# Optimization experiments

Measured on AMD Instinct MI355X. Metric: run time of the kernel, lower is better.

Reference implementation:

```python
import jax, jax.numpy as jnp
import numpy as np

NF, LF, D_E, D_R = 32, 9, 200, 200
N_ENT, B = 100000, 1024
EPS = 1e-5


def _bn(x, gamma, beta, axes):
    # training-mode batchnorm: biased variance over `axes`
    m = jnp.mean(x, axis=axes, keepdims=True)
    v = jnp.var(x, axis=axes, keepdims=True)
    return (x - m) * jax.lax.rsqrt(v + EPS) * gamma + beta


def setup_inputs() -> dict:
    key = jax.random.key(0)
    ks = jax.random.split(key, 8)
    fc1_len = NF * LF                      # 288
    fc_len = (D_E - LF + 1) * NF           # 6144
    return {
        "e1": jax.random.normal(ks[0], (B, D_E), jnp.float32),
        "r": jax.random.normal(ks[1], (B, D_R), jnp.float32),
        "fc1_w": jax.random.normal(ks[2], (fc1_len, D_R), jnp.float32) * 0.05,
        "fc1_b": jnp.zeros((fc1_len,), jnp.float32),
        "fc_w": jax.random.normal(ks[3], (D_E, fc_len), jnp.float32) * 0.02,
        "fc_b": jnp.zeros((D_E,), jnp.float32),
        "E": jax.random.normal(ks[4], (N_ENT, D_E), jnp.float32) * 0.05,
        "b": jnp.zeros((N_ENT,), jnp.float32),
        "bn0_g": jnp.ones((1,), jnp.float32),
        "bn0_b": jnp.zeros((1,), jnp.float32),
        "bn1_g": jnp.ones((NF,), jnp.float32),
        "bn1_b": jnp.zeros((NF,), jnp.float32),
        "bn2_g": jnp.ones((D_E,), jnp.float32),
        "bn2_b": jnp.zeros((D_E,), jnp.float32),
    }


def reference(e1, r, fc1_w, fc1_b, fc_w, fc_b, E, b,
              bn0_g, bn0_b, bn1_g, bn1_b, bn2_g, bn2_b):
    L = D_E - LF + 1                       # 192 output positions
    # bn0 over [B,1,d_e]: normalize across batch and length (1 channel)
    x = _bn(e1[:, None, :], bn0_g[None, :, None], bn0_b[None, :, None], (0, 2))
    x = x[:, 0, :]                         # [B, d_e]
    # hypernetwork: per-sample conv filters [B, nf, lf]
    k = (r @ fc1_w.T + fc1_b).reshape(B, NF, LF)
    # grouped conv1d (groups=B) == per-sample sliding-window contraction
    idx = jnp.arange(L)[:, None] + jnp.arange(LF)[None, :]   # [L, lf]
    Xw = x[:, idx]                          # [B, L, lf] windows
    conv = jnp.einsum('blj,bfj->bfl', Xw, k)  # [B, nf, L]
    # bn1 over channels nf
    y = _bn(conv, bn1_g[None, :, None], bn1_b[None, :, None], (0, 2))
    y = y.reshape(B, NF * L)
    y = y @ fc_w.T + fc_b                   # [B, d_e]
    y = _bn(y, bn2_g[None, :], bn2_b[None, :], (0,))
    y = jax.nn.relu(y)
    scores = y @ E.T + b                    # [B, n_ent]
    return jax.nn.sigmoid(scores)
```

## Files before the change

kernel.cpp:

```cpp
#include <hip/hip_runtime.h>
#include <math.h>

#define B_    1024
#define DE    200
#define DR    200
#define NFC   32
#define LFC   9
#define LL    192
#define FC1LEN 288
#define FCLEN 6144
#define NENT  100000
#define EPSI  1e-5f
#define KPAD  224
#define NKS   7
#define YKS   192
#define YSEG  16

#define O_S0    0
#define O_P0    64
#define O_S1    256
#define O_S2    320
#define O_P1    768
#define O_RBF   66304
#define O_W1BF  180992
#define O_K     213248
#define O_CFRAG 508160
#define O_FCWP  3653888
#define O_CVEC  4440320
#define O_PART  4440576
#define O_Y     7717376
#define O_ABF   7922176

typedef __attribute__((ext_vector_type(8))) short bf16x8;
typedef __attribute__((ext_vector_type(4))) float f32x4;

__device__ __forceinline__ float sigm(float x){
  return __fdividef(1.0f, 1.0f + __expf(-x));
}

__device__ __forceinline__ unsigned short f2bf(float f){
  unsigned int u = __float_as_uint(f);
  u = (u + 0x7FFFu + ((u >> 16) & 1u)) >> 16;
  return (unsigned short)u;
}

__device__ __forceinline__ bf16x8 pack8(float4 f0, float4 f1){
  bf16x8 o;
  o[0]=(short)f2bf(f0.x); o[1]=(short)f2bf(f0.y); o[2]=(short)f2bf(f0.z); o[3]=(short)f2bf(f0.w);
  o[4]=(short)f2bf(f1.x); o[5]=(short)f2bf(f1.y); o[6]=(short)f2bf(f1.z); o[7]=(short)f2bf(f1.w);
  return o;
}

__global__ void k_bn0_part(const float* __restrict__ e1, float* __restrict__ ws){
  __shared__ float ss[256], sq[256];
  int tid = threadIdx.x;
  float a = 0.f, b = 0.f;
  for (int i = blockIdx.x*256 + tid; i < B_*DE; i += 64*256){
    float v = e1[i]; a += v; b += v*v;
  }
  ss[tid]=a; sq[tid]=b; __syncthreads();
  for (int s=128; s>0; s>>=1){
    if (tid < s){ ss[tid]+=ss[tid+s]; sq[tid]+=sq[tid+s]; }
    __syncthreads();
  }
  if (tid==0){ ws[O_P0+2*blockIdx.x]=ss[0]; ws[O_P0+2*blockIdx.x+1]=sq[0]; }
}

__global__ void k_bn0_final(const float* __restrict__ g, const float* __restrict__ bt,
                            float* __restrict__ ws){
  int tid = threadIdx.x;
  float a = ws[O_P0+2*tid], b = ws[O_P0+2*tid+1];
  for (int o=32; o>0; o>>=1){ a += __shfl_down(a,o); b += __shfl_down(b,o); }
  if (tid==0){
    float n = (float)(B_*DE);
    float m = a/n, v = b/n - m*m;
    float s = rsqrtf(v + EPSI) * g[0];
    ws[O_S0]   = s;
    ws[O_S0+1] = bt[0] - m*s;
  }
}

__global__ void k_pack(const float* __restrict__ r, const float* __restrict__ w,
                       float* __restrict__ ws){
  int blk = blockIdx.x;
  if (blk < 112){
    int s = blk*256 + threadIdx.x;
    int lane = s & 63;
    int ks = (s >> 6) % NKS;
    int mtile = (s >> 6) / NKS;
    int m = mtile*16 + (lane & 15);
    int k0 = ks*32 + (lane >> 4)*8;
    unsigned short o8[8];
    #pragma unroll
    for (int j = 0; j < 8; ++j){
      int k = k0 + j;
      o8[j] = f2bf((k < DR) ? r[m*DR + k] : 0.f);
    }
    *(bf16x8*)((unsigned short*)(ws + O_RBF) + (size_t)s*8) = *(bf16x8*)o8;
  } else {
    int s = (blk-112)*256 + threadIdx.x;
    if (s >= 18*NKS*64) return;
    int lane = s & 63;
    int ks = (s >> 6) % NKS;
    int ntile = (s >> 6) / NKS;
    int n = ntile*16 + (lane & 15);
    int k0 = ks*32 + (lane >> 4)*8;
    unsigned short o8[8];
    #pragma unroll
    for (int j = 0; j < 8; ++j){
      int k = k0 + j;
      o8[j] = f2bf((k < DR) ? w[(size_t)n*DR + k] : 0.f);
    }
    *(bf16x8*)((unsigned short*)(ws + O_W1BF) + (size_t)s*8) = *(bf16x8*)o8;
  }
}

__global__ void k_fc1m(const float* __restrict__ bias, float* __restrict__ ws){
  const unsigned short* Rb = (const unsigned short*)(ws + O_RBF);
  const unsigned short* Wb = (const unsigned short*)(ws + O_W1BF);
  int mt = blockIdx.x;
  int nt = blockIdx.y;
  int lane = threadIdx.x;
  int lr = lane & 15, lg = lane >> 4;
  f32x4 acc[4] = {};
  #pragma unroll
  for (int ks = 0; ks < NKS; ++ks){
    bf16x8 b = *(const bf16x8*)(Wb + ((size_t)(nt*NKS + ks)*64 + lane)*8);
    #pragma unroll
    for (int mf = 0; mf < 4; ++mf){
      bf16x8 a = *(const bf16x8*)(Rb + ((size_t)((mt*4+mf)*NKS + ks)*64 + lane)*8);
      acc[mf] = __builtin_amdgcn_mfma_f32_16x16x32_bf16(a, b, acc[mf], 0, 0, 0);
    }
  }
  int col = nt*16 + lr;
  float bv = bias[col];
  #pragma unroll
  for (int mf = 0; mf < 4; ++mf){
    int row = mt*64 + mf*16 + lg*4;
    #pragma unroll
    for (int r = 0; r < 4; ++r)
      ws[O_K + (size_t)(row + r)*FC1LEN + col] = acc[mf][r] + bv;
  }
}

__global__ void k_conv(const float* __restrict__ e1, float* __restrict__ ws){
  __shared__ float xs[DE];
  __shared__ float kf[FC1LEN];
  int b = blockIdx.x, tid = threadIdx.x;
  float s0v = ws[O_S0], t0v = ws[O_S0+1];
  for (int d = tid; d < DE;     d += 256) xs[d] = e1[b*DE + d]*s0v + t0v;
  for (int i = tid; i < FC1LEN; i += 256) kf[i] = ws[O_K + (size_t)b*FC1LEN + i];
  __syncthreads();
  unsigned short* Cf = (unsigned short*)(ws + O_CFRAG);
  int f = tid >> 3, sub = tid & 7;
  int mtile = b >> 4, mlan = b & 15;
  float kr[LFC];
  #pragma unroll
  for (int j = 0; j < LFC; ++j) kr[j] = kf[f*LFC + j];
  float sum = 0.f, sq = 0.f;
  #pragma unroll
  for (int g = 0; g < 3; ++g){
    unsigned short o8[8];
    int l0 = sub*24 + g*8;
    #pragma unroll
    for (int t = 0; t < 8; ++t){
      int l = l0 + t;
      float acc = 0.f;
      #pragma unroll
      for (int j = 0; j < LFC; ++j) acc += xs[l+j]*kr[j];
      o8[t] = f2bf(acc);
      sum += acc; sq += acc*acc;
    }
    int k0 = f*LL + l0;
    int ks = k0 >> 5;
    int lane_w = ((k0 >> 3) & 3)*16 + mlan;
    size_t slot = (size_t)(mtile*YKS + ks)*64 + lane_w;
    *(bf16x8*)(Cf + slot*8) = *(bf16x8*)o8;
  }
  for (int o = 1; o < 8; o <<= 1){ sum += __shfl_xor(sum,o); sq += __shfl_xor(sq,o); }
  if (sub == 0){
    ws[O_P1 + (b*NFC + f)*2    ] = sum;
    ws[O_P1 + (b*NFC + f)*2 + 1] = sq;
  }
}

__global__ void k_bn1_final(const float* __restrict__ g, const float* __restrict__ bt,
                            float* __restrict__ ws){
  __shared__ float ss[256], sq[256];
  int f = blockIdx.x, tid = threadIdx.x;
  float a = 0.f, b = 0.f;
  for (int i = tid; i < B_; i += 256){
    a += ws[O_P1 + (i*NFC + f)*2];
    b += ws[O_P1 + (i*NFC + f)*2 + 1];
  }
  ss[tid]=a; sq[tid]=b; __syncthreads();
  for (int s=128; s>0; s>>=1){
    if (tid < s){ ss[tid]+=ss[tid+s]; sq[tid]+=sq[tid+s]; }
    __syncthreads();
  }
  if (tid==0){
    float n = (float)(B_*LL);
    float m = ss[0]/n, v = sq[0]/n - m*m;
    float s = rsqrtf(v + EPSI) * g[f];
    ws[O_S1 + f]       = s;
    ws[O_S1 + NFC + f] = bt[f] - m*s;
  }
}

__global__ void k_fcwp(const float* __restrict__ fcw, float* __restrict__ ws){
  int s = blockIdx.x*256 + threadIdx.x;
  int lane = s & 63;
  int ks = (s >> 6) % YKS;
  int ntile = (s >> 6) / YKS;
  int n = ntile*16 + (lane & 15);
  int k0 = ks*32 + (lane >> 4)*8;
  int f = (k0 >> 6) / 3;
  float sc = ws[O_S1 + f];
  unsigned short o8[8];
  if (n < DE){
    const float* p = fcw + (size_t)n*FCLEN + k0;
    float4 f0 = *(const float4*)p;
    float4 f1 = *(const float4*)(p + 4);
    o8[0]=f2bf(f0.x*sc); o8[1]=f2bf(f0.y*sc); o8[2]=f2bf(f0.z*sc); o8[3]=f2bf(f0.w*sc);
    o8[4]=f2bf(f1.x*sc); o8[5]=f2bf(f1.y*sc); o8[6]=f2bf(f1.z*sc); o8[7]=f2bf(f1.w*sc);
  } else {
    #pragma unroll
    for (int j = 0; j < 8; ++j) o8[j] = 0;
  }
  *(bf16x8*)((unsigned short*)(ws + O_FCWP) + (size_t)s*8) = *(bf16x8*)o8;
}

__global__ void k_cvec(const float* __restrict__ fcw, const float* __restrict__ fcb,
                       float* __restrict__ ws){
  __shared__ float t1s[NFC];
  __shared__ float red[256];
  int o = blockIdx.x, tid = threadIdx.x;
  if (tid < NFC) t1s[tid] = ws[O_S1 + NFC + tid];
  __syncthreads();
  float acc = 0.f;
  for (int i = tid; i < FCLEN; i += 256)
    acc += fcw[(size_t)o*FCLEN + i] * t1s[i/LL];
  red[tid] = acc; __syncthreads();
  for (int s=128; s>0; s>>=1){
    if (tid < s) red[tid] += red[tid+s];
    __syncthreads();
  }
  if (tid==0) ws[O_CVEC + o] = red[0] + fcb[o];
}

__global__ __launch_bounds__(256) void k_ygemm_m(float* __restrict__ ws){
  const unsigned short* Cb = (const unsigned short*)(ws + O_CFRAG);
  const unsigned short* Wb = (const unsigned short*)(ws + O_FCWP);
  int mt = blockIdx.x;
  int seg = blockIdx.y;
  int tid = threadIdx.x;
  int lane = tid & 63, wid = tid >> 6;
  int lr = lane & 15, lg = lane >> 4;
  f32x4 acc[4][4] = {};
  #pragma unroll 4
  for (int ksl = 0; ksl < 12; ++ksl){
    int ks = seg*12 + ksl;
    bf16x8 a[4], bfr[4];
    #pragma unroll
    for (int mf = 0; mf < 4; ++mf)
      a[mf] = *(const bf16x8*)(Cb + ((size_t)((mt*4+mf)*YKS + ks)*64 + lane)*8);
    #pragma unroll
    for (int nf = 0; nf < 4; ++nf){
      int nt = wid*4 + nf;
      bfr[nf] = *(const bf16x8*)(Wb + ((size_t)(nt*YKS + ks)*64 + lane)*8);
    }
    #pragma unroll
    for (int mf = 0; mf < 4; ++mf)
      #pragma unroll
      for (int nf = 0; nf < 4; ++nf)
        acc[mf][nf] = __builtin_amdgcn_mfma_f32_16x16x32_bf16(a[mf], bfr[nf], acc[mf][nf], 0, 0, 0);
  }
  float* part = ws + O_PART + (size_t)seg*(B_*DE);
  #pragma unroll
  for (int nf = 0; nf < 4; ++nf){
    int col = (wid*4 + nf)*16 + lr;
    if (col < DE){
      #pragma unroll
      for (int mf = 0; mf < 4; ++mf){
        int row = mt*64 + mf*16 + lg*4;
        #pragma unroll
        for (int r = 0; r < 4; ++r)
          part[(size_t)(row + r)*DE + col] = acc[mf][nf][r];
      }
    }
  }
}

__global__ void k_yreduce(float* __restrict__ ws){
  int i = blockIdx.x*256 + threadIdx.x;
  int o = i % DE;
  float y = ws[O_CVEC + o];
  #pragma unroll
  for (int s = 0; s < YSEG; ++s) y += ws[O_PART + (size_t)s*(B_*DE) + i];
  ws[O_Y + i] = y;
}

__global__ void k_bn2(const float* __restrict__ g, const float* __restrict__ bt,
                      float* __restrict__ ws){
  __shared__ float ss[256], sq[256];
  int o = blockIdx.x, tid = threadIdx.x;
  float a = 0.f, b = 0.f;
  for (int i = tid; i < B_; i += 256){
    float v = ws[O_Y + i*DE + o];
    a += v; b += v*v;
  }
  ss[tid]=a; sq[tid]=b; __syncthreads();
  for (int s=128; s>0; s>>=1){
    if (tid < s){ ss[tid]+=ss[tid+s]; sq[tid]+=sq[tid+s]; }
    __syncthreads();
  }
  if (tid==0){
    float n = (float)B_;
    float m = ss[0]/n, v = sq[0]/n - m*m;
    float s = rsqrtf(v + EPSI) * g[o];
    ws[O_S2 + o]      = s;
    ws[O_S2 + DE + o] = bt[o] - m*s;
  }
}

__global__ void k_abf(float* __restrict__ ws){
  int s = blockIdx.x*256 + threadIdx.x;
  int lane = s & 63;
  int ks = (s >> 6) % NKS;
  int mtile = (s >> 6) / NKS;
  int m = mtile*16 + (lane & 15);
  int k0 = ks*32 + (lane >> 4)*8;
  unsigned short o8[8];
  #pragma unroll
  for (int j = 0; j < 8; ++j){
    int k = k0 + j;
    float v = 0.f;
    if (k < DE){
      float y = ws[O_Y + m*DE + k];
      v = fmaxf(y*ws[O_S2 + k] + ws[O_S2 + DE + k], 0.f);
    }
    o8[j] = f2bf(v);
  }
  *(bf16x8*)((unsigned short*)(ws + O_ABF) + (size_t)s*8) = *(bf16x8*)o8;
}

__global__ __launch_bounds__(256, 2) void k_scores(const float* __restrict__ E,
                                                   const float* __restrict__ bias,
                                                   const float* __restrict__ ws,
                                                   float* __restrict__ out){
  __shared__ float tile[64*256];
  const unsigned short* Abf = (const unsigned short*)(ws + O_ABF);
  int wgid = blockIdx.x;
  int mh = wgid / 391, ns = wgid - mh*391;
  int tid = threadIdx.x;
  int lane = tid & 63, wid = tid >> 6;
  int lr = lane & 15, lg = lane >> 4;

  bf16x8 ebf[4][7];
  float bv[4];
  #pragma unroll
  for (int nf = 0; nf < 4; ++nf){
    int col = ns*256 + wid*64 + nf*16 + lr;
    int nc = (col < NENT) ? col : (NENT-1);
    bv[nf] = bias[nc];
    const float* ep = E + (size_t)nc*DE;
    #pragma unroll
    for (int ks = 0; ks < NKS; ++ks){
      int k0 = ks*32 + lg*8;
      if (k0 + 8 <= DE){
        float4 f0 = *(const float4*)(ep + k0);
        float4 f1 = *(const float4*)(ep + k0 + 4);
        ebf[nf][ks] = pack8(f0, f1);
      } else {
        ebf[nf][ks] = (bf16x8){0,0,0,0,0,0,0,0};
      }
    }
  }

  const unsigned short* aBase = Abf + (size_t)(mh*8)*1792*8 + lane*8;
  int col0 = ns*256;
  #pragma unroll 1
  for (int t = 0; t < 8; ++t){
    const unsigned short* ap = aBase + (size_t)t*1792*8;
    bf16x8 aC[4], aN[4];
    #pragma unroll
    for (int mf = 0; mf < 4; ++mf) aC[mf] = *(const bf16x8*)(ap + (size_t)(mf*NKS)*512);
    f32x4 acc[4][4] = {};
    #pragma unroll
    for (int ks = 0; ks < NKS; ++ks){
      if (ks < NKS-1){
        #pragma unroll
        for (int mf = 0; mf < 4; ++mf)
          aN[mf] = *(const bf16x8*)(ap + (size_t)(mf*NKS + ks + 1)*512);
      }
      #pragma unroll
      for (int mf = 0; mf < 4; ++mf)
        #pragma unroll
        for (int nf = 0; nf < 4; ++nf)
          acc[mf][nf] = __builtin_amdgcn_mfma_f32_16x16x32_bf16(aC[mf], ebf[nf][ks], acc[mf][nf], 0, 0, 0);
      #pragma unroll
      for (int mf = 0; mf < 4; ++mf) aC[mf] = aN[mf];
    }
    __syncthreads();
    #pragma unroll
    for (int mf = 0; mf < 4; ++mf)
      #pragma unroll
      for (int nf = 0; nf < 4; ++nf){
        int lrow = mf*16 + lg*4;
        int lcol = wid*64 + nf*16 + lr;
        #pragma unroll
        for (int r = 0; r < 4; ++r)
          tile[(lrow + r)*256 + lcol] = sigm(acc[mf][nf][r] + bv[nf]);
      }
    __syncthreads();
    int row0 = (mh*8 + t)*64;
    #pragma unroll
    for (int p = 0; p < 16; ++p){
      int lrow = p*4 + wid;
      int lcol = lane*4;
      f32x4 v = *(const f32x4*)&tile[lrow*256 + lcol];
      int gc = col0 + lcol;
      if (gc < NENT)
        __builtin_nontemporal_store(v, (f32x4*)&out[(size_t)(row0 + lrow)*NENT + gc]);
    }
  }
}

extern "C" void kernel_launch(void* const* d_in, const int* in_sizes, int n_in,
                              void* d_out, int out_size, void* d_ws, size_t ws_size,
                              hipStream_t stream){
  (void)in_sizes; (void)n_in; (void)out_size; (void)ws_size;
  const float* e1    = (const float*)d_in[0];
  const float* r     = (const float*)d_in[1];
  const float* fc1_w = (const float*)d_in[2];
  const float* fc1_b = (const float*)d_in[3];
  const float* fc_w  = (const float*)d_in[4];
  const float* fc_b  = (const float*)d_in[5];
  const float* E     = (const float*)d_in[6];
  const float* bE    = (const float*)d_in[7];
  const float* g0    = (const float*)d_in[8];
  const float* b0    = (const float*)d_in[9];
  const float* g1    = (const float*)d_in[10];
  const float* b1    = (const float*)d_in[11];
  const float* g2    = (const float*)d_in[12];
  const float* b2    = (const float*)d_in[13];
  float* ws  = (float*)d_ws;
  float* out = (float*)d_out;

  k_bn0_part  <<<64,  256, 0, stream>>>(e1, ws);
  k_bn0_final <<<1,   64,  0, stream>>>(g0, b0, ws);
  k_pack      <<<144, 256, 0, stream>>>(r, fc1_w, ws);
  k_fc1m      <<<dim3(16,18), 64, 0, stream>>>(fc1_b, ws);
  k_conv      <<<1024,256, 0, stream>>>(e1, ws);
  k_bn1_final <<<32,  256, 0, stream>>>(g1, b1, ws);
  k_fcwp      <<<768, 256, 0, stream>>>(fc_w, ws);
  k_cvec      <<<200, 256, 0, stream>>>(fc_w, fc_b, ws);
  k_ygemm_m   <<<dim3(16,16), 256, 0, stream>>>(ws);
  k_yreduce   <<<800, 256, 0, stream>>>(ws);
  k_bn2       <<<200, 256, 0, stream>>>(g2, b2, ws);
  k_abf       <<<112, 256, 0, stream>>>(ws);
  k_scores    <<<782, 256, 0, stream>>>(E, bE, ws, out);
}
```

Before: 200.9 us.

## Merge small prep kernels and give each scores block all batch rows

Folds the bn0 partial reduction into the packing kernel and merges the fc weight packing with the cvec computation, which removes two launches. The scores kernel now runs 391 blocks, each looping over all 16 row tiles instead of 8. Each block therefore converts its E slice to bf16 once instead of twice, and E is read with nontemporal loads. The cost is half as many scores workgroups, about 1.5 per CU on a 256-CU part, which may hurt load balance and latency hiding for the dominant output-write phase.

```diff
diff --git a/kernel.cpp b/kernel.cpp
--- a/kernel.cpp
+++ b/kernel.cpp
@@ -44,26 +44,59 @@
   return (unsigned short)u;
 }
 
-__device__ __forceinline__ bf16x8 pack8(float4 f0, float4 f1){
+__device__ __forceinline__ bf16x8 pack8v(f32x4 f0, f32x4 f1){
   bf16x8 o;
-  o[0]=(short)f2bf(f0.x); o[1]=(short)f2bf(f0.y); o[2]=(short)f2bf(f0.z); o[3]=(short)f2bf(f0.w);
-  o[4]=(short)f2bf(f1.x); o[5]=(short)f2bf(f1.y); o[6]=(short)f2bf(f1.z); o[7]=(short)f2bf(f1.w);
+  o[0]=(short)f2bf(f0[0]); o[1]=(short)f2bf(f0[1]); o[2]=(short)f2bf(f0[2]); o[3]=(short)f2bf(f0[3]);
+  o[4]=(short)f2bf(f1[0]); o[5]=(short)f2bf(f1[1]); o[6]=(short)f2bf(f1[2]); o[7]=(short)f2bf(f1[3]);
   return o;
 }
 
-__global__ void k_bn0_part(const float* __restrict__ e1, float* __restrict__ ws){
+__global__ void k_pack0(const float* __restrict__ r, const float* __restrict__ w,
+                        const float* __restrict__ e1, float* __restrict__ ws){
   __shared__ float ss[256], sq[256];
-  int tid = threadIdx.x;
-  float a = 0.f, b = 0.f;
-  for (int i = blockIdx.x*256 + tid; i < B_*DE; i += 64*256){
-    float v = e1[i]; a += v; b += v*v;
-  }
-  ss[tid]=a; sq[tid]=b; __syncthreads();
-  for (int s=128; s>0; s>>=1){
-    if (tid < s){ ss[tid]+=ss[tid+s]; sq[tid]+=sq[tid+s]; }
-    __syncthreads();
-  }
-  if (tid==0){ ws[O_P0+2*blockIdx.x]=ss[0]; ws[O_P0+2*blockIdx.x+1]=sq[0]; }
+  int blk = blockIdx.x;
+  if (blk < 112){
+    int s = blk*256 + threadIdx.x;
+    int lane = s & 63;
+    int ks = (s >> 6) % NKS;
+    int mtile = (s >> 6) / NKS;
+    int m = mtile*16 + (lane & 15);
+    int k0 = ks*32 + (lane >> 4)*8;
+    unsigned short o8[8];
+    #pragma unroll
+    for (int j = 0; j < 8; ++j){
+      int k = k0 + j;
+      o8[j] = f2bf((k < DR) ? r[m*DR + k] : 0.f);
+    }
+    *(bf16x8*)((unsigned short*)(ws + O_RBF) + (size_t)s*8) = *(bf16x8*)o8;
+  } else if (blk < 144){
+    int s = (blk-112)*256 + threadIdx.x;
+    if (s >= 18*NKS*64) return;
+    int lane = s & 63;
+    int ks = (s >> 6) % NKS;
+    int ntile = (s >> 6) / NKS;
+    int n = ntile*16 + (lane & 15);
+    int k0 = ks*32 + (lane >> 4)*8;
+    unsigned short o8[8];
+    #pragma unroll
+    for (int j = 0; j < 8; ++j){
+      int k = k0 + j;
+      o8[j] = f2bf((k < DR) ? w[(size_t)n*DR + k] : 0.f);
+    }
+    *(bf16x8*)((unsigned short*)(ws + O_W1BF) + (size_t)s*8) = *(bf16x8*)o8;
+  } else {
+    int bb = blk - 144, tid = threadIdx.x;
+    float a = 0.f, b = 0.f;
+    for (int i = bb*256 + tid; i < B_*DE; i += 64*256){
+      float v = e1[i]; a += v; b += v*v;
+    }
+    ss[tid]=a; sq[tid]=b; __syncthreads();
+    for (int s=128; s>0; s>>=1){
+      if (tid < s){ ss[tid]+=ss[tid+s]; sq[tid]+=sq[tid+s]; }
+      __syncthreads();
+    }
+    if (tid==0){ ws[O_P0+2*bb]=ss[0]; ws[O_P0+2*bb+1]=sq[0]; }
+  }
 }
 
 __global__ void k_bn0_final(const float* __restrict__ g, const float* __restrict__ bt,
@@ -77,41 +110,6 @@
     float s = rsqrtf(v + EPSI) * g[0];
     ws[O_S0]   = s;
     ws[O_S0+1] = bt[0] - m*s;
-  }
-}
-
-__global__ void k_pack(const float* __restrict__ r, const float* __restrict__ w,
-                       float* __restrict__ ws){
-  int blk = blockIdx.x;
-  if (blk < 112){
-    int s = blk*256 + threadIdx.x;
-    int lane = s & 63;
-    int ks = (s >> 6) % NKS;
-    int mtile = (s >> 6) / NKS;
-    int m = mtile*16 + (lane & 15);
-    int k0 = ks*32 + (lane >> 4)*8;
-    unsigned short o8[8];
-    #pragma unroll
-    for (int j = 0; j < 8; ++j){
-      int k = k0 + j;
-      o8[j] = f2bf((k < DR) ? r[m*DR + k] : 0.f);
-    }
-    *(bf16x8*)((unsigned short*)(ws + O_RBF) + (size_t)s*8) = *(bf16x8*)o8;
-  } else {
-    int s = (blk-112)*256 + threadIdx.x;
-    if (s >= 18*NKS*64) return;
-    int lane = s & 63;
-    int ks = (s >> 6) % NKS;
-    int ntile = (s >> 6) / NKS;
-    int n = ntile*16 + (lane & 15);
-    int k0 = ks*32 + (lane >> 4)*8;
-    unsigned short o8[8];
-    #pragma unroll
-    for (int j = 0; j < 8; ++j){
-      int k = k0 + j;
-      o8[j] = f2bf((k < DR) ? w[(size_t)n*DR + k] : 0.f);
-    }
-    *(bf16x8*)((unsigned short*)(ws + O_W1BF) + (size_t)s*8) = *(bf16x8*)o8;
   }
 }
 
@@ -207,45 +205,46 @@
   }
 }
 
-__global__ void k_fcwp(const float* __restrict__ fcw, float* __restrict__ ws){
-  int s = blockIdx.x*256 + threadIdx.x;
-  int lane = s & 63;
-  int ks = (s >> 6) % YKS;
-  int ntile = (s >> 6) / YKS;
-  int n = ntile*16 + (lane & 15);
-  int k0 = ks*32 + (lane >> 4)*8;
-  int f = (k0 >> 6) / 3;
-  float sc = ws[O_S1 + f];
-  unsigned short o8[8];
-  if (n < DE){
-    const float* p = fcw + (size_t)n*FCLEN + k0;
-    float4 f0 = *(const float4*)p;
-    float4 f1 = *(const float4*)(p + 4);
-    o8[0]=f2bf(f0.x*sc); o8[1]=f2bf(f0.y*sc); o8[2]=f2bf(f0.z*sc); o8[3]=f2bf(f0.w*sc);
-    o8[4]=f2bf(f1.x*sc); o8[5]=f2bf(f1.y*sc); o8[6]=f2bf(f1.z*sc); o8[7]=f2bf(f1.w*sc);
+__global__ void k_fcwp_cvec(const float* __restrict__ fcw, const float* __restrict__ fcb,
+                            float* __restrict__ ws){
+  __shared__ float shm[256];
+  int blk = blockIdx.x;
+  if (blk < 768){
+    int s = blk*256 + threadIdx.x;
+    int lane = s & 63;
+    int ks = (s >> 6) % YKS;
+    int ntile = (s >> 6) / YKS;
+    int n = ntile*16 + (lane & 15);
+    int k0 = ks*32 + (lane >> 4)*8;
+    int f = (k0 >> 6) / 3;
+    float sc = ws[O_S1 + f];
+    unsigned short o8[8];
+    if (n < DE){
+      const float* p = fcw + (size_t)n*FCLEN + k0;
+      float4 f0 = *(const float4*)p;
+      float4 f1 = *(const float4*)(p + 4);
+      o8[0]=f2bf(f0.x*sc); o8[1]=f2bf(f0.y*sc); o8[2]=f2bf(f0.z*sc); o8[3]=f2bf(f0.w*sc);
+      o8[4]=f2bf(f1.x*sc); o8[5]=f2bf(f1.y*sc); o8[6]=f2bf(f1.z*sc); o8[7]=f2bf(f1.w*sc);
+    } else {
+      #pragma unroll
+      for (int j = 0; j < 8; ++j) o8[j] = 0;
+    }
+    *(bf16x8*)((unsigned short*)(ws + O_FCWP) + (size_t)s*8) = *(bf16x8*)o8;
   } else {
-    #pragma unroll
-    for (int j = 0; j < 8; ++j) o8[j] = 0;
-  }
-  *(bf16x8*)((unsigned short*)(ws + O_FCWP) + (size_t)s*8) = *(bf16x8*)o8;
-}
-
-__global__ void k_cvec(const float* __restrict__ fcw, const float* __restrict__ fcb,
-                       float* __restrict__ ws){
-  __shared__ float t1s[NFC];
-  __shared__ float red[256];
-  int o = blockIdx.x, tid = threadIdx.x;
-  if (tid < NFC) t1s[tid] = ws[O_S1 + NFC + tid];
-  __syncthreads();
-  float acc = 0.f;
-  for (int i = tid; i < FCLEN; i += 256)
-    acc += fcw[(size_t)o*FCLEN + i] * t1s[i/LL];
-  red[tid] = acc; __syncthreads();
-  for (int s=128; s>0; s>>=1){
-    if (tid < s) red[tid] += red[tid+s];
+    __shared__ float t1s[NFC];
+    int o = blk - 768, tid = threadIdx.x;
+    if (tid < NFC) t1s[tid] = ws[O_S1 + NFC + tid];
     __syncthreads();
-  }
-  if (tid==0) ws[O_CVEC + o] = red[0] + fcb[o];
+    float acc = 0.f;
+    for (int i = tid; i < FCLEN; i += 256)
+      acc += fcw[(size_t)o*FCLEN + i] * t1s[i/LL];
+    shm[tid] = acc; __syncthreads();
+    for (int s=128; s>0; s>>=1){
+      if (tid < s) shm[tid] += shm[tid+s];
+      __syncthreads();
+    }
+    if (tid==0) ws[O_CVEC + o] = shm[0] + fcb[o];
+  }
 }
 
 __global__ __launch_bounds__(256) void k_ygemm_m(float* __restrict__ ws){
@@ -350,8 +349,7 @@
                                                    float* __restrict__ out){
   __shared__ float tile[64*256];
   const unsigned short* Abf = (const unsigned short*)(ws + O_ABF);
-  int wgid = blockIdx.x;
-  int mh = wgid / 391, ns = wgid - mh*391;
+  int ns = blockIdx.x;
   int tid = threadIdx.x;
   int lane = tid & 63, wid = tid >> 6;
   int lr = lane & 15, lg = lane >> 4;
@@ -368,19 +366,19 @@
     for (int ks = 0; ks < NKS; ++ks){
       int k0 = ks*32 + lg*8;
       if (k0 + 8 <= DE){
-        float4 f0 = *(const float4*)(ep + k0);
-        float4 f1 = *(const float4*)(ep + k0 + 4);
-        ebf[nf][ks] = pack8(f0, f1);
+        f32x4 f0 = __builtin_nontemporal_load((const f32x4*)(ep + k0));
+        f32x4 f1 = __builtin_nontemporal_load((const f32x4*)(ep + k0 + 4));
+        ebf[nf][ks] = pack8v(f0, f1);
       } else {
         ebf[nf][ks] = (bf16x8){0,0,0,0,0,0,0,0};
       }
     }
   }
 
-  const unsigned short* aBase = Abf + (size_t)(mh*8)*1792*8 + lane*8;
+  const unsigned short* aBase = Abf + lane*8;
   int col0 = ns*256;
   #pragma unroll 1
-  for (int t = 0; t < 8; ++t){
+  for (int t = 0; t < 16; ++t){
     const unsigned short* ap = aBase + (size_t)t*1792*8;
     bf16x8 aC[4], aN[4];
     #pragma unroll
@@ -413,7 +411,7 @@
           tile[(lrow + r)*256 + lcol] = sigm(acc[mf][nf][r] + bv[nf]);
       }
     __syncthreads();
-    int row0 = (mh*8 + t)*64;
+    int row0 = t*64;
     #pragma unroll
     for (int p = 0; p < 16; ++p){
       int lrow = p*4 + wid;
@@ -447,17 +445,15 @@
   float* ws  = (float*)d_ws;
   float* out = (float*)d_out;
 
-  k_bn0_part  <<<64,  256, 0, stream>>>(e1, ws);
+  k_pack0     <<<208, 256, 0, stream>>>(r, fc1_w, e1, ws);
   k_bn0_final <<<1,   64,  0, stream>>>(g0, b0, ws);
-  k_pack      <<<144, 256, 0, stream>>>(r, fc1_w, ws);
   k_fc1m      <<<dim3(16,18), 64, 0, stream>>>(fc1_b, ws);
   k_conv      <<<1024,256, 0, stream>>>(e1, ws);
   k_bn1_final <<<32,  256, 0, stream>>>(g1, b1, ws);
-  k_fcwp      <<<768, 256, 0, stream>>>(fc_w, ws);
-  k_cvec      <<<200, 256, 0, stream>>>(fc_w, fc_b, ws);
+  k_fcwp_cvec <<<968, 256, 0, stream>>>(fc_w, fc_b, ws);
   k_ygemm_m   <<<dim3(16,16), 256, 0, stream>>>(ws);
   k_yreduce   <<<800, 256, 0, stream>>>(ws);
   k_bn2       <<<200, 256, 0, stream>>>(g2, b2, ws);
   k_abf       <<<112, 256, 0, stream>>>(ws);
-  k_scores    <<<782, 256, 0, stream>>>(E, bE, ws, out);
-}
+  k_scores    <<<391, 256, 0, stream>>>(E, bE, ws, out);
+}
```

Result: no change. 197.7 us (-1.6%).
